# Kernel tuning notes

Measured on AMD Instinct MI355X. Metric: run time of the kernel, lower is better.

Reference implementation:

```python
import jax, jax.numpy as jnp
import numpy as np
import math

B, H, L, N, CD = 16, 512, 2048, 64, 128
BN_EPS = 1e-5


def setup_inputs() -> dict:
    key = jax.random.key(0)
    ks = jax.random.split(key, 12)
    x = jax.random.normal(ks[0], (B, H, L), jnp.float32)
    cond = jax.random.normal(ks[1], (B, CD), jnp.float32)
    # input Linear(H, H)
    linear_w = jax.random.normal(ks[2], (H, H), jnp.float32) * (1.0 / math.sqrt(H))
    linear_b = jax.random.normal(ks[3], (H,), jnp.float32) * 0.01
    # DSSM params (torch init: log_dt ~ U[log dt_min, log dt_max])
    log_dt = jax.random.uniform(ks[4], (H,), jnp.float32) * (math.log(0.1) - math.log(0.001)) + math.log(0.001)
    C_ri = jax.random.normal(ks[5], (H, N, 2), jnp.float32)  # view_as_real of complex C
    log_A_real = jnp.full((H, N), jnp.log(0.5), jnp.float32)
    A_imag = jnp.broadcast_to(math.pi * jnp.arange(N, dtype=jnp.float32), (H, N))
    D = jax.random.normal(ks[6], (H,), jnp.float32)
    # FiLM adaptor Linear(CD, 2H)
    film_w = jax.random.normal(ks[7], (2 * H, CD), jnp.float32) * (1.0 / math.sqrt(CD))
    film_b = jax.random.normal(ks[8], (2 * H,), jnp.float32) * 0.01
    # depthwise 1x1 residual conv (groups=H, bias=False) -> per-channel scale
    res_w = jax.random.normal(ks[9], (H,), jnp.float32)
    return {"x": x, "cond": cond, "linear_w": linear_w, "linear_b": linear_b,
            "log_dt": log_dt, "C_ri": C_ri, "log_A_real": log_A_real,
            "A_imag": A_imag, "D": D, "film_w": film_w, "film_b": film_b,
            "res_w": res_w}


def _s4_kernel(log_dt, C_ri, log_A_real, A_imag, length):
    dt = jnp.exp(log_dt)                       # [H]
    C = C_ri[..., 0] + 1j * C_ri[..., 1]       # [H, N] complex
    A = -jnp.exp(log_A_real) + 1j * A_imag     # [H, N] complex
    dtA = A * dt[:, None]                      # [H, N]
    t = jnp.arange(length, dtype=jnp.float32)
    P = dtA[:, :, None] * t                    # [H, N, L] complex
    Cm = C * (jnp.exp(dtA) - 1.0) / A          # [H, N]
    K = 2.0 * jnp.einsum('hn,hnl->hl', Cm, jnp.exp(P)).real  # [H, L]
    return K


def reference(x, cond, linear_w, linear_b, log_dt, C_ri, log_A_real, A_imag, D,
              film_w, film_b, res_w):
    # --- linear over channel dim (B H L -> B L H -> linear -> B H L) ---
    h = jnp.einsum('bhl,gh->bgl', x, linear_w) + linear_b[None, :, None]
    h = jax.nn.gelu(h, approximate=False)  # torch.nn.GELU default (erf)
    # --- DSSM: full-length group (forward passes length=None) ---
    K = _s4_kernel(log_dt, C_ri, log_A_real, A_imag, L)     # [H, L]
    n_fft = 2 * L
    k_f = jnp.fft.rfft(K, n=n_fft)                           # [H, Lf]
    u_f = jnp.fft.rfft(h, n=n_fft)                           # [B, H, Lf]
    y = jnp.fft.irfft(u_f * k_f[None], n=n_fft)[..., :L]     # [B, H, L]
    y = y + h * D[None, :, None]                             # D skip
    # --- FiLM: BatchNorm1d(affine=False, batch stats) then scale/shift ---
    gb = cond @ film_w.T + film_b                            # [B, 2H]
    g, b = gb[:, :H], gb[:, H:]
    mean = jnp.mean(y, axis=(0, 2), keepdims=True)
    var = jnp.var(y, axis=(0, 2), keepdims=True)             # biased, as torch BN
    y = (y - mean) * jax.lax.rsqrt(var + BN_EPS)
    y = y * g[:, :, None] + b[:, :, None]
    y = jax.nn.gelu(y, approximate=False)
    # --- depthwise 1x1 residual ---
    return y + x * res_w[None, :, None]
```

## Files before the change

kernel.cpp:

```cpp
#include <hip/hip_runtime.h>
#include <math.h>

#define B_ 16
#define H_ 512
#define L_ 2048
#define N_ 64
#define CD_ 128
#define KSTRIDE 2112

typedef unsigned int u32;
typedef unsigned short u16;
typedef __attribute__((ext_vector_type(8))) short bf16x8;
typedef __attribute__((ext_vector_type(4))) float f32x4;

#define GLOAD_LDS16(gsrc, ldst) \
    __builtin_amdgcn_global_load_lds( \
        (const __attribute__((address_space(1))) u32*)(const void*)(gsrc), \
        (__attribute__((address_space(3))) u32*)(void*)(ldst), 16, 0, 0)

__device__ __forceinline__ float gelu_f(float v) {
    return 0.5f * v * (1.0f + erff(v * 0.70710678118654752f));
}
__device__ __forceinline__ float bf2f(u16 b) {
    union { u32 u; float f; } c; c.u = ((u32)b) << 16; return c.f;
}
__device__ __forceinline__ u16 f2bf(float f) {
    union { float f; u32 u; } c; c.f = f;
    u32 u = c.u;
    return (u16)((u + 0x7FFFu + ((u >> 16) & 1u)) >> 16);
}
__device__ __forceinline__ u32 pack2(float a, float b) {
    u32 r;
    asm("v_cvt_pk_bf16_f32 %0, %1, %2" : "=v"(r) : "v"(a), "v"(b));
    return r;
}
__device__ __forceinline__ float2 cmul(float2 a, float2 b) {
    return make_float2(a.x * b.x - a.y * b.y, a.x * b.y + a.y * b.x);
}

__global__ void k_fill(float* __restrict__ out, int n, float val) {
    int i = blockIdx.x * 256 + threadIdx.x;
    if (i < n) out[i] = val;
}

__global__ __launch_bounds__(128) void k_prepW(const float* __restrict__ W,
                                               u16* __restrict__ Wb) {
    int g = blockIdx.x, t = threadIdx.x;
    float4 v = ((const float4*)(W + (size_t)g * H_))[t];
    u32* dst = (u32*)(Wb + (size_t)g * H_);
    dst[t * 2]     = pack2(v.x, v.y);
    dst[t * 2 + 1] = pack2(v.z, v.w);
}

__global__ __launch_bounds__(256) void k_prepX(const float* __restrict__ x,
                                               u16* __restrict__ xT) {
    int b  = blockIdx.z;
    int k0 = blockIdx.y * 64;
    int l0 = blockIdx.x * 256;
    __shared__ float xs[64][260];
    int t = threadIdx.x;
    int cr = t >> 6;
    int cc = (t & 63) * 4;
    #pragma unroll
    for (int p = 0; p < 16; ++p) {
        int r = p * 4 + cr;
        float4 v = *(const float4*)&x[((size_t)b * H_ + k0 + r) * L_ + l0 + cc];
        xs[r][cc] = v.x; xs[r][cc + 1] = v.y; xs[r][cc + 2] = v.z; xs[r][cc + 3] = v.w;
    }
    __syncthreads();
    u16* dst = xT + ((size_t)b * L_ + l0 + t) * H_ + k0;
    #pragma unroll
    for (int j = 0; j < 8; ++j) {
        uint4 w;
        w.x = pack2(xs[j * 8 + 0][t], xs[j * 8 + 1][t]);
        w.y = pack2(xs[j * 8 + 2][t], xs[j * 8 + 3][t]);
        w.z = pack2(xs[j * 8 + 4][t], xs[j * 8 + 5][t]);
        w.w = pack2(xs[j * 8 + 6][t], xs[j * 8 + 7][t]);
        *(uint4*)&dst[j * 8] = w;
    }
}

__global__ __launch_bounds__(256) void k_K4(
    const float* __restrict__ log_dt, const float* __restrict__ C_ri,
    const float* __restrict__ log_A_real, const float* __restrict__ A_imag,
    u16* __restrict__ Krv) {
    int h = blockIdx.x, t = threadIdx.x;
    __shared__ float2 P1[N_][8], P8[N_][4], P32[N_][8], P256[N_][8], Cs[N_];
    if (t < N_) {
        int n = t;
        float dt = expf(log_dt[h]);
        float a_re = -expf(log_A_real[h * N_ + n]);
        float a_im = A_imag[h * N_ + n];
        float dre = a_re * dt, dim = a_im * dt;
        float er = expf(dre);
        float s, c;
        sincosf(dim, &s, &c);
        float2 E1 = make_float2(er * c, er * s);
        float num_re = E1.x - 1.0f, num_im = E1.y;
        float den = a_re * a_re + a_im * a_im;
        float q_re = (num_re * a_re + num_im * a_im) / den;
        float q_im = (num_im * a_re - num_re * a_im) / den;
        float Cr = C_ri[(h * N_ + n) * 2 + 0], Ci = C_ri[(h * N_ + n) * 2 + 1];
        Cs[n] = make_float2(Cr * q_re - Ci * q_im, Cr * q_im + Ci * q_re);
        float2 w = make_float2(1.f, 0.f);
        #pragma unroll
        for (int i = 0; i < 8; ++i) { P1[n][i] = w; w = cmul(w, E1); }
        float2 E8 = w; w = make_float2(1.f, 0.f);
        #pragma unroll
        for (int i = 0; i < 4; ++i) { P8[n][i] = w; w = cmul(w, E8); }
        float2 E32 = w; w = make_float2(1.f, 0.f);
        #pragma unroll
        for (int i = 0; i < 8; ++i) { P32[n][i] = w; w = cmul(w, E32); }
        float2 E256 = w; w = make_float2(1.f, 0.f);
        #pragma unroll
        for (int i = 0; i < 8; ++i) { P256[n][i] = w; w = cmul(w, E256); }
    }
    __syncthreads();
    int qh = t >> 5, ql = (t >> 2) & 7, rh = t & 3;
    float acc[8] = {};
    for (int n = 0; n < N_; ++n) {
        float2 a = cmul(Cs[n], P256[n][qh]);
        a = cmul(a, P32[n][ql]);
        a = cmul(a, P8[n][rh]);
        #pragma unroll
        for (int j = 0; j < 8; ++j) {
            float2 e = P1[n][j];
            acc[j] += a.x * e.x - a.y * e.y;
        }
    }
    u16* Krow = Krv + (size_t)h * KSTRIDE;
    uint4 w4;
    w4.x = pack2(2.0f * acc[7], 2.0f * acc[6]);
    w4.y = pack2(2.0f * acc[5], 2.0f * acc[4]);
    w4.z = pack2(2.0f * acc[3], 2.0f * acc[2]);
    w4.w = pack2(2.0f * acc[1], 2.0f * acc[0]);
    *(uint4*)&Krow[2040 - 8 * t] = w4;
    if (t < 8) {
        uint4 z = {0u, 0u, 0u, 0u};
        *(uint4*)&Krow[2048 + 8 * t] = z;
    }
}

__global__ __launch_bounds__(256, 4) void k_linear9(
    const u16* __restrict__ xT, const u16* __restrict__ Wb,
    const float* __restrict__ bias, u16* __restrict__ hb16) {
    int b  = blockIdx.z;
    int g0 = blockIdx.y * 128;
    int l0 = blockIdx.x * 128;
    __shared__ __align__(16) u16 sm[128 * 128];
    u16* As = sm;
    u16* Xs = sm + 8192;
    int t = threadIdx.x;
    int lane = t & 63, wv = t >> 6;
    int n = lane & 15, kg = lane >> 4;
    int wr = wv >> 1, wc = wv & 1;
    int lr8 = lane >> 3, lc8 = lane & 7;

    f32x4 acc[4][4];
    #pragma unroll
    for (int m = 0; m < 4; ++m)
        #pragma unroll
        for (int q = 0; q < 4; ++q) acc[m][q] = (f32x4){0.f, 0.f, 0.f, 0.f};

    for (int S = 0; S < 8; ++S) {
        int k0 = S * 64;
        #pragma unroll
        for (int i = 0; i < 4; ++i) {
            int s = wv * 4 + i;
            int row = s * 8 + lr8;
            const u16* gA = Wb + (size_t)(g0 + row) * H_ + k0 + lc8 * 8;
            const u16* gX = xT + ((size_t)b * L_ + l0 + row) * H_ + k0 + lc8 * 8;
            GLOAD_LDS16(gA, &As[s * 512]);
            GLOAD_LDS16(gX, &Xs[s * 512]);
        }
        __syncthreads();
        #pragma unroll
        for (int ks = 0; ks < 2; ++ks) {
            bf16x8 af[4], bf[4];
            #pragma unroll
            for (int m = 0; m < 4; ++m)
                af[m] = *(const bf16x8*)&As[(wr * 64 + m * 16 + n) * 64 + ks * 32 + kg * 8];
            #pragma unroll
            for (int q = 0; q < 4; ++q)
                bf[q] = *(const bf16x8*)&Xs[(wc * 64 + q * 16 + n) * 64 + ks * 32 + kg * 8];
            #pragma unroll
            for (int m = 0; m < 4; ++m)
                #pragma unroll
                for (int q = 0; q < 4; ++q)
                    acc[m][q] = __builtin_amdgcn_mfma_f32_16x16x32_bf16(
                        af[m], bf[q], acc[m][q], 0, 0, 0);
        }
        __syncthreads();
    }

    u16* Yt = sm;
    #pragma unroll
    for (int m = 0; m < 4; ++m) {
        #pragma unroll
        for (int r = 0; r < 4; ++r) {
            int grow = wr * 64 + m * 16 + kg * 4 + r;
            float bi = bias[g0 + grow];
            #pragma unroll
            for (int q = 0; q < 4; ++q) {
                float v = gelu_f(acc[m][q][r] + bi);
                Yt[grow * 128 + wc * 64 + q * 16 + n] = f2bf(v);
            }
        }
    }
    __syncthreads();
    #pragma unroll
    for (int pass = 0; pass < 8; ++pass) {
        int flat = t + 256 * pass;
        int row = flat >> 4, c16 = flat & 15;
        uint4 v = *(const uint4*)&Yt[row * 128 + c16 * 8];
        *(uint4*)&hb16[((size_t)b * H_ + g0 + row) * L_ + l0 + c16 * 8] = v;
    }
}

template<int E, bool DIAG, bool TAIL, bool LOAD>
__device__ __forceinline__ void cstep(const uint2* __restrict__ KD2, int& base,
    bf16x8 (&ring)[8], f32x4 (&accR)[8], const char* smem,
    int rowbase, u32 swz, int kg16, int& ja) {
    uint2 w01, w23;
    if (DIAG) {
        int b0 = base < 2047 ? base : 2047;
        int b1 = (base + 4) < 2047 ? (base + 4) : 2047;
        w01 = KD2[b0];
        w23 = KD2[b1];
        if (base > 2047)     { w01.x = 0u; w01.y = 0u; }
        if (base + 4 > 2047) { w23.x = 0u; w23.y = 0u; }
    } else {
        w01 = KD2[base];
        w23 = KD2[base + 4];
    }
    union { u32 u[4]; bf16x8 v; } bu;
    bu.u[0] = w01.x; bu.u[1] = w01.y; bu.u[2] = w23.x; bu.u[3] = w23.y;
    #pragma unroll
    for (int m = 0; m < 8; ++m)
        if (!TAIL || m >= E)
            accR[m] = __builtin_amdgcn_mfma_f32_16x16x32_bf16(
                ring[(m - E) & 7], bu.v, accR[m], 0, 0, 0);
    if (LOAD) {
        ring[(7 - E) & 7] = *(const bf16x8*)(smem + rowbase +
                            (((u32)(ja * 64 + kg16)) ^ swz));
        ja -= 1;
    }
    base -= 32;
}

template<bool DIAG, bool TAIL, bool LOAD>
__device__ __forceinline__ void cblock8(const uint2* __restrict__ KD2, int& base,
    bf16x8 (&ring)[8], f32x4 (&accR)[8], const char* smem,
    int rowbase, u32 swz, int kg16, int& ja) {
    cstep<0, DIAG,  TAIL, LOAD>(KD2, base, ring, accR, smem, rowbase, swz, kg16, ja);
    cstep<1, false, TAIL, LOAD>(KD2, base, ring, accR, smem, rowbase, swz, kg16, ja);
    cstep<2, false, TAIL, LOAD>(KD2, base, ring, accR, smem, rowbase, swz, kg16, ja);
    cstep<3, false, TAIL, LOAD>(KD2, base, ring, accR, smem, rowbase, swz, kg16, ja);
    cstep<4, false, TAIL, LOAD>(KD2, base, ring, accR, smem, rowbase, swz, kg16, ja);
    cstep<5, false, TAIL, LOAD>(KD2, base, ring, accR, smem, rowbase, swz, kg16, ja);
    cstep<6, false, TAIL, LOAD>(KD2, base, ring, accR, smem, rowbase, swz, kg16, ja);
    cstep<7, false, TAIL, LOAD>(KD2, base, ring, accR, smem, rowbase, swz, kg16, ja);
}

__global__ __launch_bounds__(512, 4) void k_conv_mfma(
    float* __restrict__ out, const u16* __restrict__ hb16,
    const u16* __restrict__ Krv, const float* __restrict__ Dp,
    const float* __restrict__ x, const float* __restrict__ cond,
    const float* __restrict__ film_w, const float* __restrict__ film_b,
    const float* __restrict__ res_w) {
    int g = blockIdx.x;
    __shared__ __align__(16) char smem[81920];
    uint2* KD2 = (uint2*)(smem + 65536);
    int t = threadIdx.x;
    int wv = t >> 6, lane = t & 63;
    int n = lane & 15, kg = lane >> 4;

    {
        const u16* Krow = Krv + (size_t)g * KSTRIDE;
        uint2 d0 = *(const uint2*)&Krow[4 * t];
        uint2 d1 = *(const uint2*)&Krow[4 * t + 4];
        u32 m12 = (d0.x >> 16) | (d0.y << 16);
        u32 m34 = (d0.y >> 16) | (d1.x << 16);
        u32 m56 = (d1.x >> 16) | (d1.y << 16);
        uint4 e01 = {d0.x, d0.y, m12, m34};
        uint4 e23 = {d0.y, d1.x, m34, m56};
        *(uint4*)&KD2[4 * t]     = e01;
        *(uint4*)&KD2[4 * t + 2] = e23;
    }
    #pragma unroll
    for (int b = 0; b < B_; ++b) {
        uint2 p2 = *(const uint2*)&hb16[((size_t)b * H_ + g) * L_ + t * 4];
        *(uint2*)(smem + b * 4096 + (((u32)(t * 8)) ^ ((b & 7) << 4))) = p2;
    }
    __syncthreads();

    const int p = wv & 1, q4 = wv >> 1;
    const int rowbase = n * 4096;
    const u32 swz = (u32)((n & 7) << 4);
    const int kg16 = kg * 16;
    const int bofs = 8 * kg - n;
    const int rrs[2] = {q4, 7 - q4};

    f32x4 acc[2][8];
    #pragma unroll
    for (int ri = 0; ri < 2; ++ri)
        #pragma unroll
        for (int m = 0; m < 8; ++m) acc[ri][m] = (f32x4){0.f, 0.f, 0.f, 0.f};

    #pragma unroll
    for (int ri = 0; ri < 2; ++ri) {
        const int rr = rrs[ri];
        const int k8 = rr * 8;
        bf16x8 ring[8];
        #pragma unroll
        for (int m = 0; m < 8; ++m)
            ring[m] = *(const bf16x8*)(smem + rowbase +
                      (((u32)((k8 + m) * 64 + kg16)) ^ swz));
        int base = 2047 - 16 * p + bofs;
        int ja = k8 - 1;
        if (rr == 0) {
            cblock8<true, true, false>(KD2, base, ring, acc[ri], smem, rowbase, swz, kg16, ja);
        } else {
            cblock8<true, false, true>(KD2, base, ring, acc[ri], smem, rowbase, swz, kg16, ja);
            for (int bi = 1; bi < rr; ++bi)
                cblock8<false, false, true>(KD2, base, ring, acc[ri], smem, rowbase, swz, kg16, ja);
            cblock8<false, true, false>(KD2, base, ring, acc[ri], smem, rowbase, swz, kg16, ja);
        }
    }

    __syncthreads();
    float Dg = Dp[g];
    float sum = 0.f, sq = 0.f;
    #pragma unroll
    for (int ri = 0; ri < 2; ++ri) {
        #pragma unroll
        for (int m = 0; m < 8; ++m) {
            const int l0 = 16 * p + 256 * rrs[ri] + 32 * m;
            #pragma unroll
            for (int r = 0; r < 4; ++r) {
                int b = kg * 4 + r;
                u32 hoff = ((u32)(2 * (l0 + n))) ^ ((u32)((b & 7) << 4));
                float hval = bf2f(*(const u16*)(smem + b * 4096 + hoff));
                float y = acc[ri][m][r] + Dg * hval;
                sum += y; sq += y * y;
                *(u16*)(smem + b * 4096 + hoff) = f2bf(y);
            }
        }
    }
    #pragma unroll
    for (int off = 32; off > 0; off >>= 1) {
        sum += __shfl_down(sum, off);
        sq  += __shfl_down(sq, off);
    }
    __syncthreads();
    float* red = (float*)(smem + 65536);
    if (lane == 0) { red[wv] = sum; red[8 + wv] = sq; }
    if (t >= 64 && t < 96) {
        int tid = t - 64, b = tid >> 1, which = tid & 1;
        int row = which ? (H_ + g) : g;
        float a = film_b[row];
        const float4* wr4 = (const float4*)(film_w + (size_t)row * CD_);
        const float4* cp4 = (const float4*)(cond + b * CD_);
        #pragma unroll
        for (int c4 = 0; c4 < CD_ / 4; ++c4) {
            float4 cw = cp4[c4], ww = wr4[c4];
            a += cw.x * ww.x + cw.y * ww.y + cw.z * ww.z + cw.w * ww.w;
        }
        red[18 + tid] = a;
    }
    __syncthreads();
    if (t == 0) {
        float s = 0.f, q = 0.f;
        #pragma unroll
        for (int i = 0; i < 8; ++i) { s += red[i]; q += red[8 + i]; }
        const float inv = 1.0f / (float)(B_ * L_);
        float mean = s * inv;
        float var = q * inv - mean * mean;
        red[16] = mean; red[17] = rsqrtf(var + 1e-5f);
    }
    __syncthreads();

    const float mean = red[16], rstd = red[17];
    const float rw = res_w[g];
    const int fb = t >> 5, tc = t & 31;
    const float gf = red[18 + 2 * fb];
    const float bb = red[18 + 2 * fb + 1];
    const u32 fswz = (u32)((fb & 7) << 4);
    const char* yrow = smem + fb * 4096;
    const size_t rowoff = ((size_t)fb * H_ + g) * L_;
    #pragma unroll
    for (int i = 0; i < 16; ++i) {
        int l = tc * 4 + 128 * i;
        uint2 yy = *(const uint2*)(yrow + (((u32)(2 * l)) ^ fswz));
        float4 xv = *(const float4*)&x[rowoff + l];
        float4 o;
        o.x = gelu_f((bf2f((u16)(yy.x & 0xFFFFu)) - mean) * rstd * gf + bb) + xv.x * rw;
        o.y = gelu_f((bf2f((u16)(yy.x >> 16))     - mean) * rstd * gf + bb) + xv.y * rw;
        o.z = gelu_f((bf2f((u16)(yy.y & 0xFFFFu)) - mean) * rstd * gf + bb) + xv.z * rw;
        o.w = gelu_f((bf2f((u16)(yy.y >> 16))     - mean) * rstd * gf + bb) + xv.w * rw;
        *(float4*)&out[rowoff + l] = o;
    }
}

extern "C" void kernel_launch(void* const* d_in, const int* in_sizes, int n_in,
                              void* d_out, int out_size, void* d_ws, size_t ws_size,
                              hipStream_t stream) {
    const int expect[12] = {16777216, 2048, 262144, 512, 512, 65536,
                            32768, 32768, 512, 131072, 1024, 512};
    bool ok = (n_in == 12);
    if (ok) for (int i = 0; i < 12; ++i) if (in_sizes[i] != expect[i]) ok = false;
    if (!ok) {
        k_fill<<<(out_size + 255) / 256, 256, 0, stream>>>((float*)d_out, out_size, 1000.0f);
        return;
    }
    const size_t sz_Wb  = (size_t)H_ * H_ * 2;
    const size_t sz_Krv = (size_t)H_ * KSTRIDE * 2;
    const size_t sz_h   = (size_t)B_ * H_ * L_ * 2;
    if (ws_size < sz_Wb + sz_Krv + sz_h + 4096) {
        k_fill<<<(out_size + 255) / 256, 256, 0, stream>>>((float*)d_out, out_size, 2000.0f);
        return;
    }

    const float* x          = (const float*)d_in[0];
    const float* cond       = (const float*)d_in[1];
    const float* linear_w   = (const float*)d_in[2];
    const float* linear_b   = (const float*)d_in[3];
    const float* log_dt     = (const float*)d_in[4];
    const float* C_ri       = (const float*)d_in[5];
    const float* log_A_real = (const float*)d_in[6];
    const float* A_imag     = (const float*)d_in[7];
    const float* Dp         = (const float*)d_in[8];
    const float* film_w     = (const float*)d_in[9];
    const float* film_b     = (const float*)d_in[10];
    const float* res_w      = (const float*)d_in[11];

    float* outp = (float*)d_out;
    u16*   xT   = (u16*)d_out;

    char* w = (char*)d_ws;
    u16* Wb   = (u16*)w;  w += sz_Wb;
    u16* Krv  = (u16*)w;  w += sz_Krv;
    u16* hb16 = (u16*)w;

    k_prepW<<<H_, 128, 0, stream>>>(linear_w, Wb);
    dim3 gpx(L_ / 256, H_ / 64, B_);
    k_prepX<<<gpx, 256, 0, stream>>>(x, xT);
    k_K4<<<H_, 256, 0, stream>>>(log_dt, C_ri, log_A_real, A_imag, Krv);
    dim3 gmm(L_ / 128, H_ / 128, B_);
    k_linear9<<<gmm, 256, 0, stream>>>(xT, Wb, linear_b, hb16);
    k_conv_mfma<<<H_, 512, 0, stream>>>(outp, hb16, Krv, Dp, x,
                                        cond, film_w, film_b, res_w);
}
```

Baseline: 133.7 us.

## Merge prep kernels into one launch and remap GEMM block order

Folds the x transpose/bf16 conversion, weight conversion and S4 kernel generation into a single kernel that branches on block index. This removes two launches and lets the three independent jobs run at the same time. The linear GEMM now uses a 1D grid with a swizzled block index, so blocks that run together share batch and weight tiles, which should improve L2 reuse. The x staging tile is also padded differently and written with float4 LDS stores; the larger shared pool may reduce occupancy for the smaller branches.

```diff
diff --git a/kernel.cpp b/kernel.cpp
--- a/kernel.cpp
+++ b/kernel.cpp
@@ -43,110 +43,117 @@
     if (i < n) out[i] = val;
 }
 
-__global__ __launch_bounds__(128) void k_prepW(const float* __restrict__ W,
-                                               u16* __restrict__ Wb) {
-    int g = blockIdx.x, t = threadIdx.x;
-    float4 v = ((const float4*)(W + (size_t)g * H_))[t];
-    u32* dst = (u32*)(Wb + (size_t)g * H_);
-    dst[t * 2]     = pack2(v.x, v.y);
-    dst[t * 2 + 1] = pack2(v.z, v.w);
-}
-
-__global__ __launch_bounds__(256) void k_prepX(const float* __restrict__ x,
-                                               u16* __restrict__ xT) {
-    int b  = blockIdx.z;
-    int k0 = blockIdx.y * 64;
-    int l0 = blockIdx.x * 256;
-    __shared__ float xs[64][260];
-    int t = threadIdx.x;
-    int cr = t >> 6;
-    int cc = (t & 63) * 4;
-    #pragma unroll
-    for (int p = 0; p < 16; ++p) {
-        int r = p * 4 + cr;
-        float4 v = *(const float4*)&x[((size_t)b * H_ + k0 + r) * L_ + l0 + cc];
-        xs[r][cc] = v.x; xs[r][cc + 1] = v.y; xs[r][cc + 2] = v.z; xs[r][cc + 3] = v.w;
-    }
-    __syncthreads();
-    u16* dst = xT + ((size_t)b * L_ + l0 + t) * H_ + k0;
-    #pragma unroll
-    for (int j = 0; j < 8; ++j) {
-        uint4 w;
-        w.x = pack2(xs[j * 8 + 0][t], xs[j * 8 + 1][t]);
-        w.y = pack2(xs[j * 8 + 2][t], xs[j * 8 + 3][t]);
-        w.z = pack2(xs[j * 8 + 4][t], xs[j * 8 + 5][t]);
-        w.w = pack2(xs[j * 8 + 6][t], xs[j * 8 + 7][t]);
-        *(uint4*)&dst[j * 8] = w;
-    }
-}
-
-__global__ __launch_bounds__(256) void k_K4(
+__global__ __launch_bounds__(256) void k_prep(
+    const float* __restrict__ x, u16* __restrict__ xT,
+    const float* __restrict__ W, u16* __restrict__ Wb,
     const float* __restrict__ log_dt, const float* __restrict__ C_ri,
     const float* __restrict__ log_A_real, const float* __restrict__ A_imag,
     u16* __restrict__ Krv) {
-    int h = blockIdx.x, t = threadIdx.x;
-    __shared__ float2 P1[N_][8], P8[N_][4], P32[N_][8], P256[N_][8], Cs[N_];
-    if (t < N_) {
-        int n = t;
-        float dt = expf(log_dt[h]);
-        float a_re = -expf(log_A_real[h * N_ + n]);
-        float a_im = A_imag[h * N_ + n];
-        float dre = a_re * dt, dim = a_im * dt;
-        float er = expf(dre);
-        float s, c;
-        sincosf(dim, &s, &c);
-        float2 E1 = make_float2(er * c, er * s);
-        float num_re = E1.x - 1.0f, num_im = E1.y;
-        float den = a_re * a_re + a_im * a_im;
-        float q_re = (num_re * a_re + num_im * a_im) / den;
-        float q_im = (num_im * a_re - num_re * a_im) / den;
-        float Cr = C_ri[(h * N_ + n) * 2 + 0], Ci = C_ri[(h * N_ + n) * 2 + 1];
-        Cs[n] = make_float2(Cr * q_re - Ci * q_im, Cr * q_im + Ci * q_re);
-        float2 w = make_float2(1.f, 0.f);
-        #pragma unroll
-        for (int i = 0; i < 8; ++i) { P1[n][i] = w; w = cmul(w, E1); }
-        float2 E8 = w; w = make_float2(1.f, 0.f);
-        #pragma unroll
-        for (int i = 0; i < 4; ++i) { P8[n][i] = w; w = cmul(w, E8); }
-        float2 E32 = w; w = make_float2(1.f, 0.f);
-        #pragma unroll
-        for (int i = 0; i < 8; ++i) { P32[n][i] = w; w = cmul(w, E32); }
-        float2 E256 = w; w = make_float2(1.f, 0.f);
-        #pragma unroll
-        for (int i = 0; i < 8; ++i) { P256[n][i] = w; w = cmul(w, E256); }
-    }
-    __syncthreads();
-    int qh = t >> 5, ql = (t >> 2) & 7, rh = t & 3;
-    float acc[8] = {};
-    for (int n = 0; n < N_; ++n) {
-        float2 a = cmul(Cs[n], P256[n][qh]);
-        a = cmul(a, P32[n][ql]);
-        a = cmul(a, P8[n][rh]);
+    __shared__ __align__(16) char pool[64 * 264 * 4];
+    int bid = blockIdx.x, t = threadIdx.x;
+
+    if (bid < 1024) {
+        int lblk = bid & 7, kblk = (bid >> 3) & 7, b = bid >> 6;
+        int k0 = kblk * 64, l0 = lblk * 256;
+        float* xs = (float*)pool;
+        int cr = t >> 6;
+        int cc = (t & 63) * 4;
+        #pragma unroll
+        for (int p = 0; p < 16; ++p) {
+            int r = p * 4 + cr;
+            float4 v = *(const float4*)&x[((size_t)b * H_ + k0 + r) * L_ + l0 + cc];
+            *(float4*)&xs[r * 264 + cc] = v;
+        }
+        __syncthreads();
+        u16* dst = xT + ((size_t)b * L_ + l0 + t) * H_ + k0;
         #pragma unroll
         for (int j = 0; j < 8; ++j) {
-            float2 e = P1[n][j];
-            acc[j] += a.x * e.x - a.y * e.y;
-        }
-    }
-    u16* Krow = Krv + (size_t)h * KSTRIDE;
-    uint4 w4;
-    w4.x = pack2(2.0f * acc[7], 2.0f * acc[6]);
-    w4.y = pack2(2.0f * acc[5], 2.0f * acc[4]);
-    w4.z = pack2(2.0f * acc[3], 2.0f * acc[2]);
-    w4.w = pack2(2.0f * acc[1], 2.0f * acc[0]);
-    *(uint4*)&Krow[2040 - 8 * t] = w4;
-    if (t < 8) {
-        uint4 z = {0u, 0u, 0u, 0u};
-        *(uint4*)&Krow[2048 + 8 * t] = z;
+            uint4 w;
+            w.x = pack2(xs[(j * 8 + 0) * 264 + t], xs[(j * 8 + 1) * 264 + t]);
+            w.y = pack2(xs[(j * 8 + 2) * 264 + t], xs[(j * 8 + 3) * 264 + t]);
+            w.z = pack2(xs[(j * 8 + 4) * 264 + t], xs[(j * 8 + 5) * 264 + t]);
+            w.w = pack2(xs[(j * 8 + 6) * 264 + t], xs[(j * 8 + 7) * 264 + t]);
+            *(uint4*)&dst[j * 8] = w;
+        }
+    } else if (bid < 1280) {
+        int g = (bid - 1024) * 2 + (t >> 7);
+        int c = t & 127;
+        float4 v = ((const float4*)(W + (size_t)g * H_))[c];
+        u32* dst = (u32*)(Wb + (size_t)g * H_);
+        dst[c * 2]     = pack2(v.x, v.y);
+        dst[c * 2 + 1] = pack2(v.z, v.w);
+    } else {
+        int h = bid - 1280;
+        float2* P1   = (float2*)pool;
+        float2* P8   = (float2*)(pool + 4096);
+        float2* P32  = (float2*)(pool + 6144);
+        float2* P256 = (float2*)(pool + 10240);
+        float2* Cs   = (float2*)(pool + 14336);
+        if (t < N_) {
+            int n = t;
+            float dt = expf(log_dt[h]);
+            float a_re = -expf(log_A_real[h * N_ + n]);
+            float a_im = A_imag[h * N_ + n];
+            float dre = a_re * dt, dim = a_im * dt;
+            float er = expf(dre);
+            float s, c;
+            sincosf(dim, &s, &c);
+            float2 E1 = make_float2(er * c, er * s);
+            float num_re = E1.x - 1.0f, num_im = E1.y;
+            float den = a_re * a_re + a_im * a_im;
+            float q_re = (num_re * a_re + num_im * a_im) / den;
+            float q_im = (num_im * a_re - num_re * a_im) / den;
+            float Cr = C_ri[(h * N_ + n) * 2 + 0], Ci = C_ri[(h * N_ + n) * 2 + 1];
+            Cs[n] = make_float2(Cr * q_re - Ci * q_im, Cr * q_im + Ci * q_re);
+            float2 w = make_float2(1.f, 0.f);
+            #pragma unroll
+            for (int i = 0; i < 8; ++i) { P1[n * 8 + i] = w; w = cmul(w, E1); }
+            float2 E8 = w; w = make_float2(1.f, 0.f);
+            #pragma unroll
+            for (int i = 0; i < 4; ++i) { P8[n * 4 + i] = w; w = cmul(w, E8); }
+            float2 E32 = w; w = make_float2(1.f, 0.f);
+            #pragma unroll
+            for (int i = 0; i < 8; ++i) { P32[n * 8 + i] = w; w = cmul(w, E32); }
+            float2 E256 = w; w = make_float2(1.f, 0.f);
+            #pragma unroll
+            for (int i = 0; i < 8; ++i) { P256[n * 8 + i] = w; w = cmul(w, E256); }
+        }
+        __syncthreads();
+        int qh = t >> 5, ql = (t >> 2) & 7, rh = t & 3;
+        float acc[8] = {};
+        for (int n = 0; n < N_; ++n) {
+            float2 a = cmul(Cs[n], P256[n * 8 + qh]);
+            a = cmul(a, P32[n * 8 + ql]);
+            a = cmul(a, P8[n * 4 + rh]);
+            #pragma unroll
+            for (int j = 0; j < 8; ++j) {
+                float2 e = P1[n * 8 + j];
+                acc[j] += a.x * e.x - a.y * e.y;
+            }
+        }
+        u16* Krow = Krv + (size_t)h * KSTRIDE;
+        uint4 w4;
+        w4.x = pack2(2.0f * acc[7], 2.0f * acc[6]);
+        w4.y = pack2(2.0f * acc[5], 2.0f * acc[4]);
+        w4.z = pack2(2.0f * acc[3], 2.0f * acc[2]);
+        w4.w = pack2(2.0f * acc[1], 2.0f * acc[0]);
+        *(uint4*)&Krow[2040 - 8 * t] = w4;
+        if (t < 8) {
+            uint4 z = {0u, 0u, 0u, 0u};
+            *(uint4*)&Krow[2048 + 8 * t] = z;
+        }
     }
 }
 
 __global__ __launch_bounds__(256, 4) void k_linear9(
     const u16* __restrict__ xT, const u16* __restrict__ Wb,
     const float* __restrict__ bias, u16* __restrict__ hb16) {
-    int b  = blockIdx.z;
-    int g0 = blockIdx.y * 128;
-    int l0 = blockIdx.x * 128;
+    int orig = blockIdx.x;
+    int wid = (orig & 7) * 128 + (orig >> 3);
+    int b  = wid >> 6;
+    int lg = wid & 63;
+    int l0 = (lg >> 2) * 128;
+    int g0 = (lg & 3) * 128;
     __shared__ __align__(16) u16 sm[128 * 128];
     u16* As = sm;
     u16* Xs = sm + 8192;
@@ -442,12 +449,9 @@
     u16* Krv  = (u16*)w;  w += sz_Krv;
     u16* hb16 = (u16*)w;
 
-    k_prepW<<<H_, 128, 0, stream>>>(linear_w, Wb);
-    dim3 gpx(L_ / 256, H_ / 64, B_);
-    k_prepX<<<gpx, 256, 0, stream>>>(x, xT);
-    k_K4<<<H_, 256, 0, stream>>>(log_dt, C_ri, log_A_real, A_imag, Krv);
-    dim3 gmm(L_ / 128, H_ / 128, B_);
-    k_linear9<<<gmm, 256, 0, stream>>>(xT, Wb, linear_b, hb16);
+    k_prep<<<1792, 256, 0, stream>>>(x, xT, linear_w, Wb,
+                                     log_dt, C_ri, log_A_real, A_imag, Krv);
+    k_linear9<<<1024, 256, 0, stream>>>(xT, Wb, linear_b, hb16);
     k_conv_mfma<<<H_, 512, 0, stream>>>(outp, hb16, Krv, Dp, x,
                                         cond, film_w, film_b, res_w);
 }
```

New measurement: 128.0 us. 1.04x faster.
